# Kernel optimization log

Measured on AMD Instinct MI355X. Metric: run time of the kernel, lower is better.

## Reference

```python
import jax, jax.numpy as jnp
import numpy as np

D = 800  # embed dim == GRU units (hardcoded in module)


def gru_scan(x, h0, W, U, b):
    """Keras GRU, reset_after=True, activation=tanh, recurrent_activation=softmax.
    x: [B,T,D_in], h0: [B,H], W: [D_in,3H], U: [H,3H], b: [2,3H] (input bias, recurrent bias).
    Gate order: z, r, h (Keras convention). Returns (seq [B,T,H], last state [B,H])."""
    H = h0.shape[-1]
    # Precompute input projections for all timesteps (big fused GEMM).
    xg = jnp.einsum('btd,dk->btk', x, W) + b[0]          # [B,T,3H]
    xg = jnp.swapaxes(xg, 0, 1)                          # [T,B,3H]
    br = b[1]

    def step(h, xt):
        rec = h @ U + br                                 # [B,3H]
        rz, rr, rh = rec[:, :H], rec[:, H:2 * H], rec[:, 2 * H:]
        xz, xr, xh = xt[:, :H], xt[:, H:2 * H], xt[:, 2 * H:]
        z = jax.nn.softmax(xz + rz, axis=-1)             # recurrent_activation='softmax'
        r = jax.nn.softmax(xr + rr, axis=-1)
        hh = jnp.tanh(xh + r * rh)                       # reset_after: r applied after recurrent matmul
        hn = z * h + (1.0 - z) * hh
        return hn, hn

    hT, ys = jax.lax.scan(step, h0, xg)
    return jnp.swapaxes(ys, 0, 1), hT


def setup_inputs() -> dict:
    key = jax.random.key(0)
    ks = jax.random.split(key, 16)
    Vf, Ve, B, T = 30000, 32000, 64, 48
    s = 0.05

    def n(k, shape):
        return jax.random.normal(k, shape, jnp.float32) * s

    return {
        'encoder_input': jax.random.randint(ks[0], (B, T), 0, Vf),
        'decoder_input': jax.random.randint(ks[1], (B, T), 0, Ve),
        'emb_fr': n(ks[2], (Vf, D)),
        'W_d1': n(ks[3], (D, D)), 'b_d1': jnp.zeros((D,), jnp.float32),
        'Wf1': n(ks[4], (D, 3 * D)), 'Uf1': n(ks[5], (D, 3 * D)), 'bf1': jnp.zeros((2, 3 * D), jnp.float32),
        'Wf2': n(ks[6], (D, 3 * D)), 'Uf2': n(ks[7], (D, 3 * D)), 'bf2': jnp.zeros((2, 3 * D), jnp.float32),
        'emb_en': n(ks[8], (Ve, D)),
        'We1': n(ks[9], (D, 3 * D)), 'Ue1': n(ks[10], (D, 3 * D)), 'be1': jnp.zeros((2, 3 * D), jnp.float32),
        'We2': n(ks[11], (D, 3 * D)), 'Ue2': n(ks[12], (D, 3 * D)), 'be2': jnp.zeros((2, 3 * D), jnp.float32),
        'W_out': n(ks[13], (D, Ve)), 'b_out': jnp.zeros((Ve,), jnp.float32),
    }


def reference(encoder_input, decoder_input, emb_fr, W_d1, b_d1,
              Wf1, Uf1, bf1, Wf2, Uf2, bf2, emb_en,
              We1, Ue1, be1, We2, Ue2, be2, W_out, b_out):
    fe = emb_fr[encoder_input]                           # [B,Tf,D]
    fe = jax.nn.relu(fe @ W_d1 + b_d1)
    ee = emb_en[decoder_input]                           # [B,Te,D]
    B = encoder_input.shape[0]
    h0 = jnp.zeros((B, D), dtype=fe.dtype)
    g1, h1 = gru_scan(fe, h0, Wf1, Uf1, bf1)
    g2, h2 = gru_scan(g1, h1, Wf2, Uf2, bf2)
    e1, h3 = gru_scan(ee, h2, We1, Ue1, be1)
    e2, h4 = gru_scan(e1, h3, We2, Ue2, be2)
    logits = e2 @ W_out + b_out                          # [B,Te,Ve]
    return jax.nn.softmax(logits, axis=-1)
```

## Files before the change

kernel.cpp:

```cpp
#include <hip/hip_runtime.h>

#define DD 800
#define HH 800
#define BB 64
#define TT 48
#define N3H 2400
#define VV 32000
#define MR (TT*BB)
#define NBLK 25

typedef __attribute__((ext_vector_type(8))) short bf16x8;
typedef __attribute__((ext_vector_type(4))) float f32x4;
typedef __attribute__((ext_vector_type(4))) float float4v;
typedef __attribute__((address_space(1))) const unsigned int as1_uint;
typedef __attribute__((address_space(3))) unsigned int as3_uint;

__device__ __forceinline__ short f2bf(float f) {
  unsigned int u = __builtin_bit_cast(unsigned int, f);
  u = (u + 0x7fffu + ((u >> 16) & 1u)) >> 16;
  return (short)(unsigned short)u;
}

__device__ __forceinline__ void gload16(const void* g, void* l) {
  __builtin_amdgcn_global_load_lds((as1_uint*)g, (as3_uint*)l, 16, 0, 0);
}

__device__ __forceinline__ void store16_cc(short* p, bf16x8 v) {
  asm volatile("global_store_dwordx4 %0, %1, off sc0 sc1" :: "v"(p), "v"(v));
}

__global__ void k_cast_transpose(const float* __restrict__ src, short* __restrict__ dst,
                                 int K, int N) {
  __shared__ float tile[32][33];
  int n0 = blockIdx.x * 32, k0 = blockIdx.y * 32;
  int tx = threadIdx.x, ty = threadIdx.y;
#pragma unroll
  for (int i = 0; i < 4; ++i) {
    int k = k0 + ty + i * 8, n = n0 + tx;
    if (k < K && n < N) tile[ty + i * 8][tx] = src[(size_t)k * N + n];
  }
  __syncthreads();
#pragma unroll
  for (int i = 0; i < 4; ++i) {
    int n = n0 + ty + i * 8, k = k0 + tx;
    if (n < N && k < K) dst[(size_t)n * K + k] = f2bf(tile[tx][ty + i * 8]);
  }
}

__global__ void k_gather(const int* __restrict__ ids, const float* __restrict__ emb,
                         short* __restrict__ out) {
  int r = blockIdx.x;
  int t = r >> 6, b = r & 63;
  int id = ids[b * TT + t];
  int i = threadIdx.x;
  if (i < 100) {
    const float* s = emb + (size_t)id * DD + i * 8;
    float4v v0 = *(const float4v*)s;
    float4v v1 = *(const float4v*)(s + 4);
    bf16x8 o;
    o[0] = f2bf(v0[0]); o[1] = f2bf(v0[1]); o[2] = f2bf(v0[2]); o[3] = f2bf(v0[3]);
    o[4] = f2bf(v1[0]); o[5] = f2bf(v1[1]); o[6] = f2bf(v1[2]); o[7] = f2bf(v1[3]);
    *(bf16x8*)(out + (size_t)r * DD + i * 8) = o;
  }
}

template <int EPI>
__global__ __launch_bounds__(256) void k_gemm(const short* __restrict__ A,
                                              const short* __restrict__ BT,
                                              const float* __restrict__ bias,
                                              float* __restrict__ Cf,
                                              short* __restrict__ Cb,
                                              int N, int K, int ldc) {
  __shared__ short lA[128 * 32];
  __shared__ short lB[128 * 32];
  const int tid = threadIdx.x, wid = tid >> 6, lane = tid & 63;
  const int m0 = blockIdx.y * 128, n0 = blockIdx.x * 128;
  const int wr = wid >> 1, wc = wid & 1;
  f32x4 acc[4][4] = {};
  for (int kt = 0; kt < K / 32; ++kt) {
    const int kb = kt * 32;
#pragma unroll
    for (int rr = 0; rr < 2; ++rr) {
      int s = rr * 256 + tid;
      gload16(A + (size_t)(m0 + (s >> 2)) * K + kb + (s & 3) * 8, (char*)lA + s * 16);
      gload16(BT + (size_t)(n0 + (s >> 2)) * K + kb + (s & 3) * 8, (char*)lB + s * 16);
    }
    __syncthreads();
    bf16x8 af[4], bfr[4];
#pragma unroll
    for (int i = 0; i < 4; ++i)
      af[i] = *(const bf16x8*)(lA + (wr * 64 + i * 16 + (lane & 15)) * 32 + (lane >> 4) * 8);
#pragma unroll
    for (int j = 0; j < 4; ++j)
      bfr[j] = *(const bf16x8*)(lB + (wc * 64 + j * 16 + (lane & 15)) * 32 + (lane >> 4) * 8);
#pragma unroll
    for (int i = 0; i < 4; ++i)
#pragma unroll
      for (int j = 0; j < 4; ++j)
        acc[i][j] = __builtin_amdgcn_mfma_f32_16x16x32_bf16(af[i], bfr[j], acc[i][j], 0, 0, 0);
    __syncthreads();
  }
  const int hi = lane >> 4, ccol = lane & 15;
#pragma unroll
  for (int i = 0; i < 4; ++i) {
    int row = m0 + wr * 64 + i * 16 + hi * 4;
#pragma unroll
    for (int j = 0; j < 4; ++j) {
      int col = n0 + wc * 64 + j * 16 + ccol;
      if (col >= N) continue;
      float bv = bias ? bias[col] : 0.f;
#pragma unroll
      for (int rg = 0; rg < 4; ++rg) {
        int r = row + rg;
        float v = acc[i][j][rg] + bv;
        if (EPI == 0) Cf[(size_t)r * ldc + col] = v;
        else          Cb[(size_t)r * ldc + col] = f2bf(v < 0.f ? 0.f : v);
      }
    }
  }
}

__device__ __forceinline__ void bar_sync(int* flags, int ep, int tid) {
  asm volatile("s_waitcnt vmcnt(0)" ::: "memory");
  __syncthreads();
  if (tid == 0)
    __hip_atomic_store(&flags[blockIdx.x * 32], ep, __ATOMIC_RELAXED, __HIP_MEMORY_SCOPE_AGENT);
  if (tid < 64) {
    bool ok;
    do {
      int v = ep;
      if (tid < NBLK)
        v = __hip_atomic_load(&flags[tid * 32], __ATOMIC_RELAXED, __HIP_MEMORY_SCOPE_AGENT);
      ok = __all(v - ep >= 0);
      if (!ok) __builtin_amdgcn_s_sleep(1);
    } while (!ok);
  }
  __syncthreads();
}

template <int HEPI>
__global__ __launch_bounds__(512, 1) void k_fused(
    const float* __restrict__ xg, const short* __restrict__ UT,
    const float* __restrict__ br, float* __restrict__ hF,
    const short* __restrict__ hInit, short* __restrict__ hSeq,
    float* __restrict__ Spart, int* __restrict__ flags, int ep0,
    const short* __restrict__ gA, const short* __restrict__ gBT,
    const float* __restrict__ gbias, float* __restrict__ gCf,
    float* __restrict__ gPp, int gN, int gldc, int gNT, int gNtiles,
    int* __restrict__ tcnt, int pollBase) {
  __shared__ __align__(16) char smem[159744];
  const int tid = threadIdx.x, wid = tid >> 6, lane = tid & 63;
  const int hi = lane >> 4, ccol = lane & 15;

  if (blockIdx.x < NBLK) {
    short* uT    = (short*)smem;
    float* sSum  = (float*)(smem + 155136);
    short* hTile = (short*)(smem + 155648);
    const int bid = blockIdx.x, c0 = bid * 32;
    const int rt = wid & 3, ch = wid >> 2;
    for (int idx = tid; idx < 96 * 100; idx += 512) {
      int rr = idx / 100, chk = idx % 100;
      int grow = (rr >> 5) * HH + c0 + (rr & 31);
      *(bf16x8*)(uT + rr * 808 + chk * 8) = *(const bf16x8*)(UT + (size_t)grow * HH + chk * 8);
    }
    const int crow = rt * 16 + hi * 4;
    const int gcol = c0 + ch * 16 + ccol;
    const int arow = rt * 16 + ccol;
    const short* uz = uT + (0 * 32 + ch * 16 + ccol) * 808;
    const short* ur = uT + (1 * 32 + ch * 16 + ccol) * 808;
    const short* uh = uT + (2 * 32 + ch * 16 + ccol) * 808;
    f32x4 hfr;
#pragma unroll
    for (int rg = 0; rg < 4; ++rg) hfr[rg] = hF[(crow + rg) * HH + gcol];
    const float brz = br[gcol], brr = br[HH + gcol], brh = br[2 * HH + gcol];
    int ep = ep0;
    float xzv[4], xrv[4], xhv[4];
#pragma unroll
    for (int rg = 0; rg < 4; ++rg) {
      const float* xrow = xg + ((size_t)(crow + rg)) * N3H;
      xzv[rg] = xrow[gcol];
      xrv[rg] = xrow[HH + gcol];
      xhv[rg] = xrow[2 * HH + gcol];
    }
    __syncthreads();

#pragma unroll 1
    for (int t = 0; t < TT; ++t) {
      const short* hPrev = (t == 0) ? hInit : hSeq + (size_t)(t - 1) * BB * HH;
      bf16x8 areg[25];
#pragma unroll
      for (int kt = 0; kt < 25; ++kt)
        areg[kt] = *(const bf16x8*)(hPrev + arow * HH + kt * 32 + hi * 8);
      f32x4 az = {}, ar = {}, ah = {};
#pragma unroll
      for (int kt = 0; kt < 25; ++kt) {
        const int o = kt * 32 + hi * 8;
        az = __builtin_amdgcn_mfma_f32_16x16x32_bf16(areg[kt], *(const bf16x8*)(uz + o), az, 0, 0, 0);
        ar = __builtin_amdgcn_mfma_f32_16x16x32_bf16(areg[kt], *(const bf16x8*)(ur + o), ar, 0, 0, 0);
        ah = __builtin_amdgcn_mfma_f32_16x16x32_bf16(areg[kt], *(const bf16x8*)(uh + o), ah, 0, 0, 0);
      }
      float ez[4], er[4], rh[4];
      float* sb = Spart + (size_t)t * 50 * 128;
#pragma unroll
      for (int rg = 0; rg < 4; ++rg) {
        ez[rg] = __expf(xzv[rg] + az[rg] + brz);
        er[rg] = __expf(xrv[rg] + ar[rg] + brr);
        rh[rg] = ah[rg] + brh;
        float s1 = ez[rg], s2 = er[rg];
#pragma unroll
        for (int mm = 1; mm < 16; mm <<= 1) {
          s1 += __shfl_xor(s1, mm);
          s2 += __shfl_xor(s2, mm);
        }
        if (ccol == 0) {
          const int slot = bid * 2 + ch;
          __hip_atomic_store(&sb[slot * 128 + crow + rg], s1, __ATOMIC_RELAXED, __HIP_MEMORY_SCOPE_AGENT);
          __hip_atomic_store(&sb[slot * 128 + 64 + crow + rg], s2, __ATOMIC_RELAXED, __HIP_MEMORY_SCOPE_AGENT);
        }
      }
      bar_sync(flags, ++ep, tid);
      if (tid < 128) {
        float s = 0.f;
#pragma unroll
        for (int sl = 0; sl < 2 * NBLK; ++sl)
          s += __hip_atomic_load(&sb[sl * 128 + tid], __ATOMIC_RELAXED, __HIP_MEMORY_SCOPE_AGENT);
        sSum[tid] = s;
      }
      __syncthreads();
#pragma unroll
      for (int rg = 0; rg < 4; ++rg) {
        int r = crow + rg;
        float z = ez[rg] / sSum[r];
        float rr2 = er[rg] / sSum[64 + r];
        float hh = tanhf(xhv[rg] + rr2 * rh[rg]);
        float hn = z * hfr[rg] + (1.f - z) * hh;
        hfr[rg] = hn;
        hTile[r * 32 + ch * 16 + ccol] = f2bf(hn);
      }
      __syncthreads();
      short* hCur = hSeq + (size_t)t * BB * HH;
      if (tid < 256) {
        int row = tid >> 2, seg = tid & 3;
        store16_cc(hCur + row * HH + c0 + seg * 8, *(const bf16x8*)(hTile + row * 32 + seg * 8));
      }
      if (t + 1 < TT) {
#pragma unroll
        for (int rg = 0; rg < 4; ++rg) {
          const float* xrow = xg + ((size_t)(t + 1) * BB + crow + rg) * N3H;
          xzv[rg] = xrow[gcol];
          xrv[rg] = xrow[HH + gcol];
          xhv[rg] = xrow[2 * HH + gcol];
        }
      }
      bar_sync(flags, ++ep, tid);
    }
#pragma unroll
    for (int rg = 0; rg < 4; ++rg) hF[(crow + rg) * HH + gcol] = hfr[rg];
    return;
  }

  short* lA = (short*)smem;
  short* lB = (short*)(smem + 40960);
  int*   tk = (int*)(smem + 81920);
  const int wr = wid >> 1, wc = wid & 1;
  for (;;) {
    if (tid == 0)
      tk[0] = __hip_atomic_fetch_add(tcnt, 1, __ATOMIC_RELAXED, __HIP_MEMORY_SCOPE_AGENT);
    __syncthreads();
    const int t0 = tk[0];
    if (t0 >= gNtiles) break;
    int mb, nb;
    if (HEPI == 2) {
      if (t0 < 2500)      { int r2 = t0;        nb = r2 / 10; mb = 0  + r2 % 10; }
      else if (t0 < 4500) { int r2 = t0 - 2500; nb = r2 / 8;  mb = 10 + r2 % 8;  }
      else if (t0 < 5500) { int r2 = t0 - 4500; nb = r2 / 4;  mb = 18 + r2 % 4;  }
      else                { int r2 = t0 - 5500; nb = r2 / 2;  mb = 22 + r2 % 2;  }
    } else {
      mb = t0 / gNT; nb = t0 % gNT;
    }
    const int m0 = mb * 128, n0 = nb * 128;
    {
      int tmax = 2 * mb + 1; if (tmax > TT - 1) tmax = TT - 1;
      const int ft = pollBase + 2 * tmax + 2;
      bool ok;
      do {
        int v = ft;
        if (lane < NBLK)
          v = __hip_atomic_load(&flags[lane * 32], __ATOMIC_RELAXED, __HIP_MEMORY_SCOPE_AGENT);
        ok = __all(v - ft >= 0);
        if (!ok) __builtin_amdgcn_s_sleep(2);
      } while (!ok);
      asm volatile("" ::: "memory");
    }
    f32x4 acc[2][4] = {};
#pragma unroll 1
    for (int kt = 0; kt < 5; ++kt) {
      const int kb = kt * 160;
#pragma unroll
      for (int i = 0; i < 5; ++i) {
        int c = tid + 512 * i;
        int row = c / 20, seg = c % 20;
        gload16(gA + (size_t)(m0 + row) * 800 + kb + seg * 8, (char*)lA + c * 16);
        gload16(gBT + (size_t)(n0 + row) * 800 + kb + seg * 8, (char*)lB + c * 16);
      }
      __syncthreads();
#pragma unroll
      for (int kk = 0; kk < 5; ++kk) {
        bf16x8 af[2], bf[4];
#pragma unroll
        for (int i = 0; i < 2; ++i)
          af[i] = *(const bf16x8*)(lA + (wr * 32 + i * 16 + (lane & 15)) * 160 + kk * 32 + hi * 8);
#pragma unroll
        for (int j = 0; j < 4; ++j)
          bf[j] = *(const bf16x8*)(lB + (wc * 64 + j * 16 + (lane & 15)) * 160 + kk * 32 + hi * 8);
#pragma unroll
        for (int i = 0; i < 2; ++i)
#pragma unroll
          for (int j = 0; j < 4; ++j)
            acc[i][j] = __builtin_amdgcn_mfma_f32_16x16x32_bf16(af[i], bf[j], acc[i][j], 0, 0, 0);
      }
      __syncthreads();
    }
    if (HEPI == 2) {
#pragma unroll
      for (int i = 0; i < 2; ++i) {
        int row = m0 + wr * 32 + i * 16 + hi * 4;
#pragma unroll
        for (int rg = 0; rg < 4; ++rg) {
          int r = row + rg;
          int orow = (r & 63) * TT + (r >> 6);
          float part = 0.f;
#pragma unroll
          for (int j = 0; j < 4; ++j) {
            int col = n0 + wc * 64 + j * 16 + ccol;
            float v = __expf(acc[i][j][rg] + gbias[col]);
            part += v;
            __builtin_nontemporal_store(v, &gCf[(size_t)orow * gldc + col]);
          }
#pragma unroll
          for (int mm = 1; mm < 16; mm <<= 1) part += __shfl_xor(part, mm);
          if (ccol == 0) __builtin_nontemporal_store(part, &gPp[(size_t)orow * 512 + nb * 2 + wc]);
        }
      }
    } else {
#pragma unroll
      for (int i = 0; i < 2; ++i) {
        int row = m0 + wr * 32 + i * 16 + hi * 4;
#pragma unroll
        for (int j = 0; j < 4; ++j) {
          int col = n0 + wc * 64 + j * 16 + ccol;
          if (col >= gN) continue;
          float bv = gbias[col];
#pragma unroll
          for (int rg = 0; rg < 4; ++rg)
            gCf[(size_t)(row + rg) * gldc + col] = acc[i][j][rg] + bv;
        }
      }
    }
  }
}

__global__ __launch_bounds__(256) void k_softmax(float* __restrict__ out,
                                                 const float* __restrict__ Pp) {
  float* row = out + (size_t)blockIdx.x * VV;
  const float* pp = Pp + (size_t)blockIdx.x * 512;
  const int tid = threadIdx.x;
  __shared__ float red[4];
  float sum = 0.f;
  for (int i = tid; i < 500; i += 256) sum += pp[i];
#pragma unroll
  for (int s = 32; s >= 1; s >>= 1) sum += __shfl_xor(sum, s);
  if ((tid & 63) == 0) red[tid >> 6] = sum;
  __syncthreads();
  float inv = 1.f / (red[0] + red[1] + red[2] + red[3]);
  for (int i = tid * 4; i < VV; i += 1024) {
    float4v v = *(const float4v*)(row + i);
    v[0] *= inv; v[1] *= inv; v[2] *= inv; v[3] *= inv;
    *(float4v*)(row + i) = v;
  }
}

extern "C" void kernel_launch(void* const* d_in, const int* in_sizes, int n_in,
                              void* d_out, int out_size, void* d_ws, size_t ws_size,
                              hipStream_t stream) {
  (void)in_sizes; (void)n_in; (void)out_size; (void)ws_size;
  const int*   enc  = (const int*)d_in[0];
  const int*   dec  = (const int*)d_in[1];
  const float* embF = (const float*)d_in[2];
  const float* Wd1  = (const float*)d_in[3];
  const float* bd1  = (const float*)d_in[4];
  const float* Wf1  = (const float*)d_in[5];
  const float* Uf1  = (const float*)d_in[6];
  const float* bf1  = (const float*)d_in[7];
  const float* Wf2  = (const float*)d_in[8];
  const float* Uf2  = (const float*)d_in[9];
  const float* bf2  = (const float*)d_in[10];
  const float* embE = (const float*)d_in[11];
  const float* We1  = (const float*)d_in[12];
  const float* Ue1  = (const float*)d_in[13];
  const float* be1  = (const float*)d_in[14];
  const float* We2  = (const float*)d_in[15];
  const float* Ue2  = (const float*)d_in[16];
  const float* be2  = (const float*)d_in[17];
  const float* Wout = (const float*)d_in[18];
  const float* bout = (const float*)d_in[19];

  char* p = (char*)d_ws;
  auto alloc = [&](size_t bytes) { char* r = p; p += (bytes + 255) & ~(size_t)255; return r; };
  short* WdT = (short*)alloc((size_t)896 * 800 * 2);
  short* WTb[4]; short* UTb[4];
  for (int i = 0; i < 4; ++i) {
    WTb[i] = (short*)alloc((size_t)2432 * 800 * 2);
    UTb[i] = (short*)alloc((size_t)2400 * 800 * 2);
  }
  short* WoT = (short*)alloc((size_t)VV * 800 * 2);
  short* feA = (short*)alloc((size_t)MR * DD * 2);
  short* fe  = (short*)alloc((size_t)MR * DD * 2);
  short* ee  = (short*)alloc((size_t)MR * DD * 2);
  short* g1  = (short*)alloc((size_t)MR * HH * 2);
  short* g2s = (short*)alloc((size_t)MR * HH * 2);
  short* e1  = (short*)alloc((size_t)MR * HH * 2);
  short* e2  = (short*)alloc((size_t)MR * HH * 2);
  float* xgA = (float*)alloc((size_t)MR * N3H * 4);
  float* xgB = (float*)alloc((size_t)MR * N3H * 4);
  float* Ppart = (float*)alloc((size_t)MR * 512 * 4);
  float* Spart = (float*)alloc((size_t)TT * 50 * 128 * 4);
  float* hF   = (float*)alloc((size_t)BB * HH * 4);
  short* hIn0 = (short*)alloc((size_t)BB * HH * 2);
  int* flags  = (int*)alloc((size_t)NBLK * 32 * 4);
  int* tcnt   = (int*)alloc((size_t)16 * 4);

  size_t tail = (char*)(tcnt + 16) - (char*)hF;
  hipMemsetAsync(hF, 0, tail, stream);

  dim3 tb(32, 8);
  k_cast_transpose<<<dim3(25, 25), tb, 0, stream>>>(Wd1, WdT, 800, 800);
  const float* Ws[4] = {Wf1, Wf2, We1, We2};
  const float* Us[4] = {Uf1, Uf2, Ue1, Ue2};
  for (int i = 0; i < 4; ++i) {
    k_cast_transpose<<<dim3(75, 25), tb, 0, stream>>>(Ws[i], WTb[i], 800, 2400);
    k_cast_transpose<<<dim3(75, 25), tb, 0, stream>>>(Us[i], UTb[i], 800, 2400);
  }
  k_cast_transpose<<<dim3(1000, 25), tb, 0, stream>>>(Wout, WoT, 800, VV);
  k_gather<<<MR, 128, 0, stream>>>(enc, embF, feA);
  k_gather<<<MR, 128, 0, stream>>>(dec, embE, ee);
  k_gemm<1><<<dim3(7, 24), 256, 0, stream>>>(feA, WdT, bd1, nullptr, fe, 800, 800, 800);
  k_gemm<0><<<dim3(19, 24), 256, 0, stream>>>(fe, WTb[0], bf1, xgA, nullptr, N3H, 800, N3H);

  const float* bs[4] = {bf1, bf2, be1, be2};
  short* hSeqL[4] = {g1, g2s, e1, e2};
  float* xgR[4] = {xgA, xgB, xgA, xgB};
  const short* hA[4]   = {g1, ee, e1, e2};
  const short* hBT[4]  = {WTb[1], WTb[2], WTb[3], WoT};
  const float* hBias[4]= {bs[1], bs[2], bs[3], bout};
  float* hOut[4] = {xgB, xgA, xgB, (float*)d_out};
  int   hPoll[4] = {0 * 96, -1000000, 2 * 96, 3 * 96};

  for (int l = 0; l < 4; ++l) {
    const short* hInit = (l == 0) ? hIn0 : hSeqL[l - 1] + (size_t)(TT - 1) * BB * HH;
    if (l < 3) {
      k_fused<0><<<256, 512, 0, stream>>>(xgR[l], UTb[l], bs[l] + N3H, hF, hInit, hSeqL[l],
                                          Spart, flags, l * 2 * TT,
                                          hA[l], hBT[l], hBias[l], hOut[l], nullptr,
                                          N3H, N3H, 19, 24 * 19, &tcnt[l], hPoll[l]);
    } else {
      k_fused<2><<<256, 512, 0, stream>>>(xgR[l], UTb[l], bs[l] + N3H, hF, hInit, hSeqL[l],
                                          Spart, flags, l * 2 * TT,
                                          hA[l], hBT[l], hBias[l], hOut[l], Ppart,
                                          VV, VV, 250, 24 * 250, &tcnt[l], hPoll[l]);
    }
  }
  k_softmax<<<MR, 256, 0, stream>>>((float*)d_out, Ppart);
}
```

Before: 2.271 ms.

## Store exp logits as bf16 in output buffer and batch weight casts

The output-projection epilogue now writes exp(logit) as bf16 into the first half of each row's output region instead of fp32. The softmax kernel reads those bf16 values back, walking chunks from high to low with a barrier so in-place fp32 writes never overwrite unread bf16 data, then normalizes. This roughly halves the write traffic of the large logits pass and the read traffic of the normalize pass, at the cost of bf16 rounding before normalization. Separately, eight weight cast-transpose launches are merged into one 3D-grid launch to cut launch overhead.

```diff
diff --git a/kernel.cpp b/kernel.cpp
--- a/kernel.cpp
+++ b/kernel.cpp
@@ -10,6 +10,7 @@
 #define NBLK 25
 
 typedef __attribute__((ext_vector_type(8))) short bf16x8;
+typedef __attribute__((ext_vector_type(4))) short short4v;
 typedef __attribute__((ext_vector_type(4))) float f32x4;
 typedef __attribute__((ext_vector_type(4))) float float4v;
 typedef __attribute__((address_space(1))) const unsigned int as1_uint;
@@ -20,6 +21,9 @@
   u = (u + 0x7fffu + ((u >> 16) & 1u)) >> 16;
   return (short)(unsigned short)u;
 }
+__device__ __forceinline__ float bf2f(short s) {
+  return __builtin_bit_cast(float, (unsigned int)(unsigned short)s << 16);
+}
 
 __device__ __forceinline__ void gload16(const void* g, void* l) {
   __builtin_amdgcn_global_load_lds((as1_uint*)g, (as3_uint*)l, 16, 0, 0);
@@ -29,8 +33,9 @@
   asm volatile("global_store_dwordx4 %0, %1, off sc0 sc1" :: "v"(p), "v"(v));
 }
 
-__global__ void k_cast_transpose(const float* __restrict__ src, short* __restrict__ dst,
-                                 int K, int N) {
+__device__ __forceinline__ void cast_transpose_body(const float* __restrict__ src,
+                                                    short* __restrict__ dst,
+                                                    int K, int N) {
   __shared__ float tile[32][33];
   int n0 = blockIdx.x * 32, k0 = blockIdx.y * 32;
   int tx = threadIdx.x, ty = threadIdx.y;
@@ -45,6 +50,16 @@
     int n = n0 + ty + i * 8, k = k0 + tx;
     if (n < N && k < K) dst[(size_t)n * K + k] = f2bf(tile[tx][ty + i * 8]);
   }
+}
+
+__global__ void k_cast_transpose(const float* __restrict__ src, short* __restrict__ dst,
+                                 int K, int N) {
+  cast_transpose_body(src, dst, K, N);
+}
+
+struct CastBatch { const float* src[8]; short* dst[8]; };
+__global__ void k_cast8(CastBatch cb) {
+  cast_transpose_body(cb.src[blockIdx.z], cb.dst[blockIdx.z], 800, 2400);
 }
 
 __global__ void k_gather(const int* __restrict__ ids, const float* __restrict__ emb,
@@ -322,6 +337,7 @@
       __syncthreads();
     }
     if (HEPI == 2) {
+      short* eb = (short*)gCf;
 #pragma unroll
       for (int i = 0; i < 2; ++i) {
         int row = m0 + wr * 32 + i * 16 + hi * 4;
@@ -335,7 +351,7 @@
             int col = n0 + wc * 64 + j * 16 + ccol;
             float v = __expf(acc[i][j][rg] + gbias[col]);
             part += v;
-            __builtin_nontemporal_store(v, &gCf[(size_t)orow * gldc + col]);
+            __builtin_nontemporal_store(f2bf(v), &eb[(size_t)orow * 2 * VV + col]);
           }
 #pragma unroll
           for (int mm = 1; mm < 16; mm <<= 1) part += __shfl_xor(part, mm);
@@ -362,7 +378,9 @@
 
 __global__ __launch_bounds__(256) void k_softmax(float* __restrict__ out,
                                                  const float* __restrict__ Pp) {
-  float* row = out + (size_t)blockIdx.x * VV;
+  const size_t base = (size_t)blockIdx.x * VV;
+  float* row = out + base;
+  const short* eb = (const short*)out + 2 * base;
   const float* pp = Pp + (size_t)blockIdx.x * 512;
   const int tid = threadIdx.x;
   __shared__ float red[4];
@@ -373,10 +391,19 @@
   if ((tid & 63) == 0) red[tid >> 6] = sum;
   __syncthreads();
   float inv = 1.f / (red[0] + red[1] + red[2] + red[3]);
-  for (int i = tid * 4; i < VV; i += 1024) {
-    float4v v = *(const float4v*)(row + i);
-    v[0] *= inv; v[1] *= inv; v[2] *= inv; v[3] *= inv;
-    *(float4v*)(row + i) = v;
+#pragma unroll 1
+  for (int j = 31; j >= 0; --j) {
+    int i = j * 1024 + tid * 4;
+    bool act = (i < VV);
+    short4v v = {};
+    if (act) v = *(const short4v*)(eb + i);
+    __syncthreads();
+    if (act) {
+      float4v o;
+      o[0] = bf2f(v[0]) * inv; o[1] = bf2f(v[1]) * inv;
+      o[2] = bf2f(v[2]) * inv; o[3] = bf2f(v[3]) * inv;
+      *(float4v*)(row + i) = o;
+    }
   }
 }
 
@@ -435,12 +462,12 @@
 
   dim3 tb(32, 8);
   k_cast_transpose<<<dim3(25, 25), tb, 0, stream>>>(Wd1, WdT, 800, 800);
-  const float* Ws[4] = {Wf1, Wf2, We1, We2};
-  const float* Us[4] = {Uf1, Uf2, Ue1, Ue2};
-  for (int i = 0; i < 4; ++i) {
-    k_cast_transpose<<<dim3(75, 25), tb, 0, stream>>>(Ws[i], WTb[i], 800, 2400);
-    k_cast_transpose<<<dim3(75, 25), tb, 0, stream>>>(Us[i], UTb[i], 800, 2400);
-  }
+  CastBatch cb;
+  cb.src[0] = Wf1; cb.src[1] = Wf2; cb.src[2] = We1; cb.src[3] = We2;
+  cb.src[4] = Uf1; cb.src[5] = Uf2; cb.src[6] = Ue1; cb.src[7] = Ue2;
+  cb.dst[0] = WTb[0]; cb.dst[1] = WTb[1]; cb.dst[2] = WTb[2]; cb.dst[3] = WTb[3];
+  cb.dst[4] = UTb[0]; cb.dst[5] = UTb[1]; cb.dst[6] = UTb[2]; cb.dst[7] = UTb[3];
+  k_cast8<<<dim3(75, 25, 8), tb, 0, stream>>>(cb);
   k_cast_transpose<<<dim3(1000, 25), tb, 0, stream>>>(Wout, WoT, 800, VV);
   k_gather<<<MR, 128, 0, stream>>>(enc, embF, feA);
   k_gather<<<MR, 128, 0, stream>>>(dec, embE, ee);
```

Result: faster. 2.208 ms (-2.8%).
